# Kernel optimization log

Measured on AMD Instinct MI355X. Metric: run time of the kernel, lower is better.

The kernel has to match this reference:

```python
import jax, jax.numpy as jnp
import numpy as np

D_MODEL, N_HEADS, D_FF = 1024, 16, 4096
SCALE = 0.1          # lookup-activation input quantization step
NUM_BITS = 8
LEVELS = 1 << NUM_BITS   # 256
HALF = LEVELS // 2       # 128
MAX_EXP = 4
EPS = 1e-5


def pow2_weight(key, shape, max_exp=MAX_EXP):
    """Ternary power-of-two weights: values in {0, +/-2^{-e}}, e in [max_exp, max_exp+3].
    Exponent range keeps fan-in-1024 outputs O(1)."""
    k1, k2 = jax.random.split(key)
    sign = jax.random.randint(k1, shape, -1, 2).astype(jnp.float32)  # {-1,0,1}
    e = jax.random.randint(k2, shape, max_exp, max_exp + 4).astype(jnp.float32)
    return sign * jnp.exp2(-e)


def setup_inputs() -> dict:
    key = jax.random.key(0)
    ks = jax.random.split(key, 8)
    x = jax.random.normal(ks[0], (4, 2048, D_MODEL), dtype=jnp.float32)
    return {
        "x": x,
        "ln1_g": jnp.ones((D_MODEL,), jnp.float32),
        "ln1_b": jnp.zeros((D_MODEL,), jnp.float32),
        "wq": pow2_weight(ks[1], (D_MODEL, D_MODEL)),
        "wk": pow2_weight(ks[2], (D_MODEL, D_MODEL)),
        "wv": pow2_weight(ks[3], (D_MODEL, D_MODEL)),
        "wo": pow2_weight(ks[4], (D_MODEL, D_MODEL)),
        "ln2_g": jnp.ones((D_MODEL,), jnp.float32),
        "ln2_b": jnp.zeros((D_MODEL,), jnp.float32),
        "w1": pow2_weight(ks[5], (D_MODEL, D_FF)),
        "w2": pow2_weight(ks[6], (D_FF, D_MODEL)),
    }


def _layernorm(x, g, b):
    mu = jnp.mean(x, axis=-1, keepdims=True)
    var = jnp.var(x, axis=-1, keepdims=True)
    return (x - mu) * jax.lax.rsqrt(var + EPS) * g + b


def _lookup_act(x):
    # StructuredLookupActivation: quantize input to 2^num_bits levels, gather from
    # a precomputed GELU table (proved via Lasso lookup in the SNARK).
    grid = (jnp.arange(LEVELS, dtype=jnp.float32) - HALF) * SCALE
    table = jax.nn.gelu(grid)
    idx = jnp.clip(jnp.round(x / SCALE).astype(jnp.int32) + HALF, 0, LEVELS - 1)
    return table[idx]


def _linear_attention(x, wq, wk, wv, wo):
    B, S, D = x.shape
    H, Dh = N_HEADS, D // N_HEADS
    q = (x @ wq).reshape(B, S, H, Dh)
    k = (x @ wk).reshape(B, S, H, Dh)
    v = (x @ wv).reshape(B, S, H, Dh)
    # elu+1 feature map -> O(S*Dh^2) linear attention (no [S,S] scores)
    phi_q = jax.nn.elu(q) + 1.0
    phi_k = jax.nn.elu(k) + 1.0
    kv = jnp.einsum('bshd,bshe->bhde', phi_k, v)          # [B,H,Dh,Dh]
    z = jnp.sum(phi_k, axis=1)                            # [B,H,Dh]
    num = jnp.einsum('bshd,bhde->bshe', phi_q, kv)        # [B,S,H,Dh]
    den = jnp.einsum('bshd,bhd->bsh', phi_q, z)[..., None] + 1e-6
    out = (num / den).reshape(B, S, D)
    return out @ wo


def reference(x, ln1_g, ln1_b, wq, wk, wv, wo, ln2_g, ln2_b, w1, w2):
    # norm -> linear attention -> residual
    x = x + _linear_attention(_layernorm(x, ln1_g, ln1_b), wq, wk, wv, wo)
    # norm -> ternary FFN with lookup activation -> residual
    h = _layernorm(x, ln2_g, ln2_b)
    x = x + (_lookup_act(h @ w1) @ w2)
    return x
```

## Files before the change

### kernel.cpp

```cpp
#include <hip/hip_runtime.h>
#include <cstdint>
#include <cstddef>


#define D_MODEL 1024
#define SEQ     2048
#define BATCH   4
#define NTOK    8192
#define NHEADS  16
#define DH      64
#define DFF     4096
#define KVCH    16
#define CHROWS  (SEQ / KVCH)
#define PSTRIDE 4160

typedef _Float16 half8 __attribute__((ext_vector_type(8)));
typedef float f32x4 __attribute__((ext_vector_type(4)));

__device__ __forceinline__ unsigned short f2h(float x) {
  _Float16 h = (_Float16)x;
  union { _Float16 h; unsigned short u; } c; c.h = h; return c.u;
}

__device__ __forceinline__ float phi_act(float x) {
  return x > 0.f ? x + 1.f : expf(x);
}

__device__ __forceinline__ float gelu_exact(float v) {
  float c = 0.7978845608028654f;
  float t = tanhf(c * (v + 0.044715f * v * v * v));
  return 0.5f * v * (1.f + t);
}

__device__ __forceinline__ void gl_lds16(const void* g, void* l) {
  __builtin_amdgcn_global_load_lds(
      (const __attribute__((address_space(1))) unsigned int*)g,
      (__attribute__((address_space(3))) unsigned int*)l, 16, 0, 0);
}

__global__ __launch_bounds__(256) void convT(const float* __restrict__ W,
                                             unsigned short* __restrict__ WT,
                                             int K, int N) {
  __shared__ float tile[64][65];
  int kb = blockIdx.y << 6, nb = blockIdx.x << 6;
  int t = threadIdx.x;
  int rr = t >> 4, cc = (t & 15) << 2;
#pragma unroll
  for (int i = 0; i < 4; ++i) {
    int r = rr + (i << 4);
    float4 v = *(const float4*)(W + (size_t)(kb + r) * N + nb + cc);
    tile[r][cc] = v.x; tile[r][cc + 1] = v.y; tile[r][cc + 2] = v.z; tile[r][cc + 3] = v.w;
  }
  __syncthreads();
#pragma unroll
  for (int i = 0; i < 4; ++i) {
    int n = rr + (i << 4);
    ushort4 o;
    o.x = f2h(tile[cc + 0][n]); o.y = f2h(tile[cc + 1][n]);
    o.z = f2h(tile[cc + 2][n]); o.w = f2h(tile[cc + 3][n]);
    *(ushort4*)(WT + (size_t)(nb + n) * K + kb + cc) = o;
  }
}

__global__ __launch_bounds__(256) void ln_kernel(const float* __restrict__ X,
                                                 const float* __restrict__ g,
                                                 const float* __restrict__ b,
                                                 unsigned short* __restrict__ Y) {
  int tok = blockIdx.x;
  int t = threadIdx.x;
  const float4* xr = (const float4*)(X + (size_t)tok * D_MODEL);
  float4 v = xr[t];
  float s  = v.x + v.y + v.z + v.w;
  float s2 = v.x * v.x + v.y * v.y + v.z * v.z + v.w * v.w;
#pragma unroll
  for (int o = 32; o > 0; o >>= 1) {
    s  += __shfl_down(s, o);
    s2 += __shfl_down(s2, o);
  }
  __shared__ float red[8];
  __shared__ float mu_s, rs_s;
  int wid = t >> 6;
  if ((t & 63) == 0) { red[wid] = s; red[wid + 4] = s2; }
  __syncthreads();
  if (t == 0) {
    float ts  = red[0] + red[1] + red[2] + red[3];
    float ts2 = red[4] + red[5] + red[6] + red[7];
    float mu  = ts * (1.f / D_MODEL);
    float var = ts2 * (1.f / D_MODEL) - mu * mu;
    mu_s = mu;
    rs_s = rsqrtf(var + 1e-5f);
  }
  __syncthreads();
  float mu = mu_s, rs = rs_s;
  float4 gv = ((const float4*)g)[t];
  float4 bv = ((const float4*)b)[t];
  ushort4 hv;
  hv.x = f2h((v.x - mu) * rs * gv.x + bv.x);
  hv.y = f2h((v.y - mu) * rs * gv.y + bv.y);
  hv.z = f2h((v.z - mu) * rs * gv.z + bv.z);
  hv.w = f2h((v.w - mu) * rs * gv.w + bv.w);
  ((ushort4*)(Y + (size_t)tok * D_MODEL))[t] = hv;
}

template <int EP>
__global__ __launch_bounds__(256, 4) void mfma_gemm(
    const unsigned short* __restrict__ A,
    const unsigned short* __restrict__ BT,
    void* Cv, const float* R, int N, int K) {
  __shared__ unsigned short smem[2 * 8192];
  __shared__ float gtab[EP == 3 ? 256 : 1];
  unsigned short* sA = smem;
  unsigned short* sB = smem + 8192;

  int t = threadIdx.x;
  if (EP == 3) gtab[t & 255] = gelu_exact((float)((t & 255) - 128) * 0.1f);

  int bm, bn;
  {
    int L = blockIdx.y * gridDim.x + blockIdx.x;
    if ((gridDim.y & 7) == 0) {
      int xcd = L & 7, wi = L >> 3;
      int mPerX = gridDim.y >> 3;
      bm = xcd * mPerX + wi / gridDim.x;
      bn = wi % gridDim.x;
    } else {
      bn = blockIdx.x; bm = blockIdx.y;
    }
  }

  int w = t >> 6, l = t & 63;
  int rl = l >> 3, cl = l & 7;
  int gseg = (cl ^ rl) << 4;
  int m0 = bm << 7;
  int n0 = bn << 7;
  size_t strideB = (size_t)K * 2;

  const char* gA[4]; const char* gB[4];
  int ldsOff[4];
  for (int j = 0; j < 4; ++j) {
    int row = (w << 5) + (j << 3) + rl;
    gA[j] = (const char*)A + (size_t)(m0 + row) * strideB + gseg;
    gB[j] = (const char*)BT + (size_t)(n0 + row) * strideB + gseg;
    ldsOff[j] = ((w << 5) + (j << 3)) << 6;
  }

  int wm = w >> 1, wn = w & 1;
  int m16 = l & 15, qd = l >> 4;

  f32x4 acc[4][4];
#pragma unroll
  for (int i = 0; i < 4; ++i)
#pragma unroll
    for (int j = 0; j < 4; ++j) acc[i][j] = (f32x4){0.f, 0.f, 0.f, 0.f};

  for (int k0 = 0; k0 < K; k0 += 64) {
    size_t kb = (size_t)k0 * 2;
#pragma unroll
    for (int j = 0; j < 4; ++j) {
      gl_lds16(gA[j] + kb, sA + ldsOff[j]);
      gl_lds16(gB[j] + kb, sB + ldsOff[j]);
    }
    __syncthreads();
#pragma unroll
    for (int kk = 0; kk < 2; ++kk) {
      int ksb = (kk << 2) + qd;
      half8 af[4], bf[4];
#pragma unroll
      for (int mt = 0; mt < 4; ++mt) {
        int r = (wm << 6) + (mt << 4) + m16;
        int slot = ksb ^ (r & 7);
        af[mt] = *(const half8*)(sA + (r << 6) + (slot << 3));
      }
#pragma unroll
      for (int nt = 0; nt < 4; ++nt) {
        int r = (wn << 6) + (nt << 4) + m16;
        int slot = ksb ^ (r & 7);
        bf[nt] = *(const half8*)(sB + (r << 6) + (slot << 3));
      }
#pragma unroll
      for (int mt = 0; mt < 4; ++mt)
#pragma unroll
        for (int nt = 0; nt < 4; ++nt)
          acc[mt][nt] = __builtin_amdgcn_mfma_f32_16x16x32_f16(af[mt], bf[nt], acc[mt][nt], 0, 0, 0);
    }
    __syncthreads();
  }

  int colBase = n0 + (wn << 6) + m16;
#pragma unroll
  for (int mt = 0; mt < 4; ++mt) {
    int rBase = m0 + (wm << 6) + (mt << 4) + (qd << 2);
#pragma unroll
    for (int nt = 0; nt < 4; ++nt) {
      int col = colBase + (nt << 4);
#pragma unroll
      for (int i = 0; i < 4; ++i) {
        size_t idx = (size_t)(rBase + i) * N + col;
        float v = acc[mt][nt][i];
        if (EP == 1)      ((float*)Cv)[idx] = phi_act(v);
        else if (EP == 2) ((float*)Cv)[idx] = R[idx] + v;
        else if (EP == 3) {
          float r = rintf(v / 0.1f);
          int iq = (int)r + 128;
          iq = iq < 0 ? 0 : (iq > 255 ? 255 : iq);
          ((unsigned short*)Cv)[idx] = f2h(gtab[iq]);
        } else            ((float*)Cv)[idx] = v;
      }
    }
  }
}

__global__ __launch_bounds__(256) void kvz_partial(const float* __restrict__ PK,
                                                   const float* __restrict__ V,
                                                   float* __restrict__ P) {
  int c = blockIdx.x, bh = blockIdx.y;
  int b = bh >> 4, h = bh & 15;
  __shared__ float pk[8][64];
  __shared__ float vv[8][64];
  int t = threadIdx.x;
  const size_t base = ((size_t)b * SEQ + (size_t)c * CHROWS) * D_MODEL + h * DH;
  int u = t & 127;
  int lrow = u >> 4;
  int lcol = (u & 15) << 2;
  bool isV = (t >= 128);
  const float* src = isV ? V : PK;
  int dkb = (t >> 4) << 2;
  int deb = (t & 15) << 2;
  float acc[4][4] = {};
  float zacc = 0.f;
  for (int s0 = 0; s0 < CHROWS; s0 += 8) {
    float4 ld = *(const float4*)(src + base + (size_t)(s0 + lrow) * D_MODEL + lcol);
    __syncthreads();
    if (isV) *(float4*)&vv[lrow][lcol] = ld;
    else     *(float4*)&pk[lrow][lcol] = ld;
    __syncthreads();
#pragma unroll
    for (int ss = 0; ss < 8; ++ss) {
      float4 a  = *(const float4*)&pk[ss][dkb];
      float4 bb = *(const float4*)&vv[ss][deb];
      acc[0][0] += a.x * bb.x; acc[0][1] += a.x * bb.y; acc[0][2] += a.x * bb.z; acc[0][3] += a.x * bb.w;
      acc[1][0] += a.y * bb.x; acc[1][1] += a.y * bb.y; acc[1][2] += a.y * bb.z; acc[1][3] += a.y * bb.w;
      acc[2][0] += a.z * bb.x; acc[2][1] += a.z * bb.y; acc[2][2] += a.z * bb.z; acc[2][3] += a.z * bb.w;
      acc[3][0] += a.w * bb.x; acc[3][1] += a.w * bb.y; acc[3][2] += a.w * bb.z; acc[3][3] += a.w * bb.w;
    }
    if (t < 64) {
#pragma unroll
      for (int ss = 0; ss < 8; ++ss) zacc += pk[ss][t];
    }
  }
  float* Pb = P + ((size_t)c * 64 + bh) * PSTRIDE;
#pragma unroll
  for (int i = 0; i < 4; ++i) {
    float4 o; o.x = acc[i][0]; o.y = acc[i][1]; o.z = acc[i][2]; o.w = acc[i][3];
    *(float4*)(Pb + (size_t)(dkb + i) * DH + deb) = o;
  }
  if (t < 64) Pb[4096 + t] = zacc;
}

__global__ __launch_bounds__(256) void kvz_reduce(const float* __restrict__ P,
                                                  float* __restrict__ KV,
                                                  float* __restrict__ Z) {
  int bh = blockIdx.x;
  int t = threadIdx.x;
  for (int i = t; i < PSTRIDE; i += 256) {
    float s = 0.f;
#pragma unroll
    for (int c = 0; c < KVCH; ++c)
      s += P[((size_t)c * 64 + bh) * PSTRIDE + i];
    if (i < 4096) KV[(size_t)bh * 4096 + i] = s;
    else          Z[(size_t)bh * 64 + (i - 4096)] = s;
  }
}

__global__ __launch_bounds__(256) void attn_kernel(const float* __restrict__ PQ,
                                                   const float* __restrict__ KVm,
                                                   const float* __restrict__ Z,
                                                   unsigned short* __restrict__ O) {
  int s0 = blockIdx.x << 6;
  int h = blockIdx.y, b = blockIdx.z;
  __shared__ float Pqt[64][64];
  __shared__ float Kv[64][64];
  __shared__ float den[64];
  __shared__ float zsh[64];
  int t = threadIdx.x;
  size_t qbase  = ((size_t)b * SEQ + s0) * D_MODEL + h * DH;
  size_t kvbase = (size_t)(b * NHEADS + h) * (DH * DH);
  int r0 = t >> 4;
  int c4 = (t & 15) << 2;
#pragma unroll
  for (int rr = 0; rr < 4; ++rr) {
    int row = r0 + (rr << 4);
    *(float4*)&Kv[row][c4] = *(const float4*)(KVm + kvbase + (size_t)row * DH + c4);
    float4 q = *(const float4*)(PQ + qbase + (size_t)row * D_MODEL + c4);
    Pqt[c4 + 0][row] = q.x;
    Pqt[c4 + 1][row] = q.y;
    Pqt[c4 + 2][row] = q.z;
    Pqt[c4 + 3][row] = q.w;
  }
  if (t < 16) *(float4*)&zsh[t << 2] = *(const float4*)(Z + (size_t)(b * NHEADS + h) * DH + (t << 2));
  __syncthreads();
  if (t < 64) {
    float d_ = 1e-6f;
#pragma unroll
    for (int dd = 0; dd < 64; ++dd) d_ += Pqt[dd][t] * zsh[dd];
    den[t] = d_;
  }
  __syncthreads();
  int tokb = (t >> 4) << 2, eb = (t & 15) << 2;
  float acc[4][4] = {};
#pragma unroll 8
  for (int dd = 0; dd < 64; ++dd) {
    float4 a  = *(const float4*)&Pqt[dd][tokb];
    float4 bb = *(const float4*)&Kv[dd][eb];
    acc[0][0] += a.x * bb.x; acc[0][1] += a.x * bb.y; acc[0][2] += a.x * bb.z; acc[0][3] += a.x * bb.w;
    acc[1][0] += a.y * bb.x; acc[1][1] += a.y * bb.y; acc[1][2] += a.y * bb.z; acc[1][3] += a.y * bb.w;
    acc[2][0] += a.z * bb.x; acc[2][1] += a.z * bb.y; acc[2][2] += a.z * bb.z; acc[2][3] += a.z * bb.w;
    acc[3][0] += a.w * bb.x; acc[3][1] += a.w * bb.y; acc[3][2] += a.w * bb.z; acc[3][3] += a.w * bb.w;
  }
#pragma unroll
  for (int i = 0; i < 4; ++i) {
    float dv = den[tokb + i];
    ushort4 hv;
    hv.x = f2h(acc[i][0] / dv);
    hv.y = f2h(acc[i][1] / dv);
    hv.z = f2h(acc[i][2] / dv);
    hv.w = f2h(acc[i][3] / dv);
    size_t oidx = ((size_t)b * SEQ + s0 + tokb + i) * D_MODEL + h * DH + eb;
    *(ushort4*)(O + oidx) = hv;
  }
}

extern "C" void kernel_launch(void* const* d_in, const int* in_sizes, int n_in,
                              void* d_out, int out_size, void* d_ws, size_t ws_size,
                              hipStream_t stream) {
  const float* x    = (const float*)d_in[0];
  const float* ln1g = (const float*)d_in[1];
  const float* ln1b = (const float*)d_in[2];
  const float* wq   = (const float*)d_in[3];
  const float* wk   = (const float*)d_in[4];
  const float* wv   = (const float*)d_in[5];
  const float* wo   = (const float*)d_in[6];
  const float* ln2g = (const float*)d_in[7];
  const float* ln2b = (const float*)d_in[8];
  const float* w1   = (const float*)d_in[9];
  const float* w2   = (const float*)d_in[10];
  float* out = (float*)d_out;
  char* ws = (char*)d_ws;

  const size_t MB = 1024 * 1024;
  unsigned short* xn   = (unsigned short*)(ws);
  float*          phiq = (float*)(ws + 32 * MB);
  float*          phik = (float*)(ws + 64 * MB);
  float*          vbuf = (float*)(ws + 96 * MB);
  unsigned short* ffn  = (unsigned short*)(ws + 32 * MB);
  unsigned short* w1T  = (unsigned short*)(ws + 96 * MB);
  unsigned short* w2T  = (unsigned short*)(ws + 104 * MB);
  unsigned short* woT  = (unsigned short*)(ws + 128 * MB);

  unsigned short* wqT = (unsigned short*)d_out;
  unsigned short* wkT = wqT + (size_t)D_MODEL * D_MODEL;
  unsigned short* wvT = wkT + (size_t)D_MODEL * D_MODEL;
  float* kvP = (float*)((char*)d_out + 6 * MB);
  float* kv  = (float*)((char*)d_out + 24 * MB);
  float* z   = (float*)((char*)d_out + 25 * MB);

  dim3 blk(256);
  dim3 gcD(D_MODEL / 64, D_MODEL / 64);

  convT<<<gcD, blk, 0, stream>>>(wq, wqT, D_MODEL, D_MODEL);
  convT<<<gcD, blk, 0, stream>>>(wk, wkT, D_MODEL, D_MODEL);
  convT<<<gcD, blk, 0, stream>>>(wv, wvT, D_MODEL, D_MODEL);
  convT<<<gcD, blk, 0, stream>>>(wo, woT, D_MODEL, D_MODEL);

  ln_kernel<<<NTOK, blk, 0, stream>>>(x, ln1g, ln1b, xn);

  dim3 gD(D_MODEL / 128, NTOK / 128);
  mfma_gemm<1><<<gD, blk, 0, stream>>>(xn, wqT, phiq, nullptr, D_MODEL, D_MODEL);
  mfma_gemm<1><<<gD, blk, 0, stream>>>(xn, wkT, phik, nullptr, D_MODEL, D_MODEL);
  mfma_gemm<0><<<gD, blk, 0, stream>>>(xn, wvT, vbuf, nullptr, D_MODEL, D_MODEL);

  kvz_partial<<<dim3(KVCH, BATCH * NHEADS), blk, 0, stream>>>(phik, vbuf, kvP);
  kvz_reduce<<<BATCH * NHEADS, blk, 0, stream>>>(kvP, kv, z);

  attn_kernel<<<dim3(SEQ / 64, NHEADS, BATCH), blk, 0, stream>>>(phiq, kv, z, xn);

  convT<<<dim3(DFF / 64, D_MODEL / 64), blk, 0, stream>>>(w1, w1T, D_MODEL, DFF);
  convT<<<dim3(D_MODEL / 64, DFF / 64), blk, 0, stream>>>(w2, w2T, DFF, D_MODEL);

  mfma_gemm<2><<<gD, blk, 0, stream>>>(xn, woT, out, x, D_MODEL, D_MODEL);

  ln_kernel<<<NTOK, blk, 0, stream>>>(out, ln2g, ln2b, xn);

  dim3 gF(DFF / 128, NTOK / 128);
  mfma_gemm<3><<<gF, blk, 0, stream>>>(xn, w1T, ffn, nullptr, DFF, D_MODEL);

  mfma_gemm<2><<<gD, blk, 0, stream>>>(ffn, w2T, out, out, D_MODEL, DFF);
}
```

Before: 496.9 us.

## Fuse Q/K/V projections into one GEMM and store activations as fp16

The three separate Q, K and V projection GEMMs become one GEMM over a concatenated transposed weight. A new epilogue routes each 1024-column slab to its own buffer, applies the elu+1 feature map to the Q and K slabs, and writes fp16 instead of fp32. The linear-attention kernels now read fp16 inputs, which halves their activation traffic and removes two launches. The cost is fp16 rounding of phi_q, phi_k and v before the kv reduction, which could reduce accuracy.

Result: faster. 482.5 us (-2.9%).

```diff
diff --git a/kernel.cpp b/kernel.cpp
--- a/kernel.cpp
+++ b/kernel.cpp
@@ -20,6 +20,9 @@
 __device__ __forceinline__ unsigned short f2h(float x) {
   _Float16 h = (_Float16)x;
   union { _Float16 h; unsigned short u; } c; c.h = h; return c.u;
+}
+__device__ __forceinline__ float h2f(unsigned short u) {
+  union { unsigned short u; _Float16 h; } c; c.u = u; return (float)c.h;
 }
 
 __device__ __forceinline__ float phi_act(float x) {
@@ -186,6 +189,10 @@
     __syncthreads();
   }
 
+  int sel = n0 >> 10;
+  size_t slab = (size_t)sel * ((size_t)NTOK * D_MODEL);
+  int colL = (n0 & 1023) + (wn << 6) + m16;
+
   int colBase = n0 + (wn << 6) + m16;
 #pragma unroll
   for (int mt = 0; mt < 4; ++mt) {
@@ -195,23 +202,28 @@
       int col = colBase + (nt << 4);
 #pragma unroll
       for (int i = 0; i < 4; ++i) {
-        size_t idx = (size_t)(rBase + i) * N + col;
         float v = acc[mt][nt][i];
-        if (EP == 1)      ((float*)Cv)[idx] = phi_act(v);
-        else if (EP == 2) ((float*)Cv)[idx] = R[idx] + v;
-        else if (EP == 3) {
-          float r = rintf(v / 0.1f);
-          int iq = (int)r + 128;
-          iq = iq < 0 ? 0 : (iq > 255 ? 255 : iq);
-          ((unsigned short*)Cv)[idx] = f2h(gtab[iq]);
-        } else            ((float*)Cv)[idx] = v;
+        if (EP == 4) {
+          if (sel < 2) v = phi_act(v);
+          size_t idx = slab + (size_t)(rBase + i) * D_MODEL + colL + (nt << 4);
+          ((unsigned short*)Cv)[idx] = f2h(v);
+        } else {
+          size_t idx = (size_t)(rBase + i) * N + col;
+          if (EP == 2)      ((float*)Cv)[idx] = R[idx] + v;
+          else if (EP == 3) {
+            float r = rintf(v / 0.1f);
+            int iq = (int)r + 128;
+            iq = iq < 0 ? 0 : (iq > 255 ? 255 : iq);
+            ((unsigned short*)Cv)[idx] = f2h(gtab[iq]);
+          } else          ((float*)Cv)[idx] = v;
+        }
       }
     }
   }
 }
 
-__global__ __launch_bounds__(256) void kvz_partial(const float* __restrict__ PK,
-                                                   const float* __restrict__ V,
+__global__ __launch_bounds__(256) void kvz_partial(const unsigned short* __restrict__ PK,
+                                                   const unsigned short* __restrict__ V,
                                                    float* __restrict__ P) {
   int c = blockIdx.x, bh = blockIdx.y;
   int b = bh >> 4, h = bh & 15;
@@ -223,16 +235,17 @@
   int lrow = u >> 4;
   int lcol = (u & 15) << 2;
   bool isV = (t >= 128);
-  const float* src = isV ? V : PK;
+  const unsigned short* src = isV ? V : PK;
   int dkb = (t >> 4) << 2;
   int deb = (t & 15) << 2;
   float acc[4][4] = {};
   float zacc = 0.f;
   for (int s0 = 0; s0 < CHROWS; s0 += 8) {
-    float4 ld = *(const float4*)(src + base + (size_t)(s0 + lrow) * D_MODEL + lcol);
+    ushort4 ld = *(const ushort4*)(src + base + (size_t)(s0 + lrow) * D_MODEL + lcol);
+    float f0 = h2f(ld.x), f1 = h2f(ld.y), f2 = h2f(ld.z), f3 = h2f(ld.w);
     __syncthreads();
-    if (isV) *(float4*)&vv[lrow][lcol] = ld;
-    else     *(float4*)&pk[lrow][lcol] = ld;
+    if (isV) { vv[lrow][lcol] = f0; vv[lrow][lcol+1] = f1; vv[lrow][lcol+2] = f2; vv[lrow][lcol+3] = f3; }
+    else     { pk[lrow][lcol] = f0; pk[lrow][lcol+1] = f1; pk[lrow][lcol+2] = f2; pk[lrow][lcol+3] = f3; }
     __syncthreads();
 #pragma unroll
     for (int ss = 0; ss < 8; ++ss) {
@@ -272,7 +285,7 @@
   }
 }
 
-__global__ __launch_bounds__(256) void attn_kernel(const float* __restrict__ PQ,
+__global__ __launch_bounds__(256) void attn_kernel(const unsigned short* __restrict__ PQ,
                                                    const float* __restrict__ KVm,
                                                    const float* __restrict__ Z,
                                                    unsigned short* __restrict__ O) {
@@ -291,11 +304,11 @@
   for (int rr = 0; rr < 4; ++rr) {
     int row = r0 + (rr << 4);
     *(float4*)&Kv[row][c4] = *(const float4*)(KVm + kvbase + (size_t)row * DH + c4);
-    float4 q = *(const float4*)(PQ + qbase + (size_t)row * D_MODEL + c4);
-    Pqt[c4 + 0][row] = q.x;
-    Pqt[c4 + 1][row] = q.y;
-    Pqt[c4 + 2][row] = q.z;
-    Pqt[c4 + 3][row] = q.w;
+    ushort4 q = *(const ushort4*)(PQ + qbase + (size_t)row * D_MODEL + c4);
+    Pqt[c4 + 0][row] = h2f(q.x);
+    Pqt[c4 + 1][row] = h2f(q.y);
+    Pqt[c4 + 2][row] = h2f(q.z);
+    Pqt[c4 + 3][row] = h2f(q.w);
   }
   if (t < 16) *(float4*)&zsh[t << 2] = *(const float4*)(Z + (size_t)(b * NHEADS + h) * DH + (t << 2));
   __syncthreads();
@@ -349,17 +362,16 @@
 
   const size_t MB = 1024 * 1024;
   unsigned short* xn   = (unsigned short*)(ws);
-  float*          phiq = (float*)(ws + 32 * MB);
-  float*          phik = (float*)(ws + 64 * MB);
-  float*          vbuf = (float*)(ws + 96 * MB);
+  unsigned short* qkv  = (unsigned short*)(ws + 32 * MB);
+  unsigned short* phiq = qkv;
+  unsigned short* phik = qkv + (size_t)NTOK * D_MODEL;
+  unsigned short* vbuf = qkv + 2 * (size_t)NTOK * D_MODEL;
   unsigned short* ffn  = (unsigned short*)(ws + 32 * MB);
   unsigned short* w1T  = (unsigned short*)(ws + 96 * MB);
   unsigned short* w2T  = (unsigned short*)(ws + 104 * MB);
   unsigned short* woT  = (unsigned short*)(ws + 128 * MB);
 
-  unsigned short* wqT = (unsigned short*)d_out;
-  unsigned short* wkT = wqT + (size_t)D_MODEL * D_MODEL;
-  unsigned short* wvT = wkT + (size_t)D_MODEL * D_MODEL;
+  unsigned short* wqkvT = (unsigned short*)d_out;
   float* kvP = (float*)((char*)d_out + 6 * MB);
   float* kv  = (float*)((char*)d_out + 24 * MB);
   float* z   = (float*)((char*)d_out + 25 * MB);
@@ -367,17 +379,15 @@
   dim3 blk(256);
   dim3 gcD(D_MODEL / 64, D_MODEL / 64);
 
-  convT<<<gcD, blk, 0, stream>>>(wq, wqT, D_MODEL, D_MODEL);
-  convT<<<gcD, blk, 0, stream>>>(wk, wkT, D_MODEL, D_MODEL);
-  convT<<<gcD, blk, 0, stream>>>(wv, wvT, D_MODEL, D_MODEL);
+  convT<<<gcD, blk, 0, stream>>>(wq, wqkvT, D_MODEL, D_MODEL);
+  convT<<<gcD, blk, 0, stream>>>(wk, wqkvT + (size_t)D_MODEL * D_MODEL, D_MODEL, D_MODEL);
+  convT<<<gcD, blk, 0, stream>>>(wv, wqkvT + 2 * (size_t)D_MODEL * D_MODEL, D_MODEL, D_MODEL);
   convT<<<gcD, blk, 0, stream>>>(wo, woT, D_MODEL, D_MODEL);
 
   ln_kernel<<<NTOK, blk, 0, stream>>>(x, ln1g, ln1b, xn);
 
-  dim3 gD(D_MODEL / 128, NTOK / 128);
-  mfma_gemm<1><<<gD, blk, 0, stream>>>(xn, wqT, phiq, nullptr, D_MODEL, D_MODEL);
-  mfma_gemm<1><<<gD, blk, 0, stream>>>(xn, wkT, phik, nullptr, D_MODEL, D_MODEL);
-  mfma_gemm<0><<<gD, blk, 0, stream>>>(xn, wvT, vbuf, nullptr, D_MODEL, D_MODEL);
+  dim3 gQKV(3 * D_MODEL / 128, NTOK / 128);
+  mfma_gemm<4><<<gQKV, blk, 0, stream>>>(xn, wqkvT, qkv, nullptr, 3 * D_MODEL, D_MODEL);
 
   kvz_partial<<<dim3(KVCH, BATCH * NHEADS), blk, 0, stream>>>(phik, vbuf, kvP);
   kvz_reduce<<<BATCH * NHEADS, blk, 0, stream>>>(kvP, kv, z);
@@ -387,6 +397,7 @@
   convT<<<dim3(DFF / 64, D_MODEL / 64), blk, 0, stream>>>(w1, w1T, D_MODEL, DFF);
   convT<<<dim3(D_MODEL / 64, DFF / 64), blk, 0, stream>>>(w2, w2T, DFF, D_MODEL);
 
+  dim3 gD(D_MODEL / 128, NTOK / 128);
   mfma_gemm<2><<<gD, blk, 0, stream>>>(xn, woT, out, x, D_MODEL, D_MODEL);
 
   ln_kernel<<<NTOK, blk, 0, stream>>>(out, ln2g, ln2b, xn);
```
